# Optimization experiments

Measured on AMD Instinct MI355X. Metric: run time of the kernel, lower is better.

Reference implementation:

```python
import jax, jax.numpy as jnp
import numpy as np

EPS = 1e-5


def _bn_linear(x, g, b, W, c, relu):
    # BatchNorm1d over flattened (B*N) axis with batch statistics (training mode),
    # then Linear, then optional ReLU. x: [B, N, Din]
    mean = jnp.mean(x, axis=(0, 1))
    var = jnp.mean(jnp.square(x - mean), axis=(0, 1))  # biased variance, as torch BN uses in fwd
    xn = (x - mean) * jax.lax.rsqrt(var + EPS) * g + b
    y = jnp.einsum('bnd,od->bno', xn, W) + c
    return jax.nn.relu(y) if relu else y


def setup_inputs() -> dict:
    key = jax.random.key(0)
    ks = jax.random.split(key, 8)
    B, N = 32, 2048
    dims = [256, 512, 512, 1024]  # in_size, hidden_sizes..., out_size
    inp = {"set_feats": jax.random.normal(ks[0], (B, N, dims[0]), dtype=jnp.float32)}
    for i, (din, dout) in enumerate(zip(dims[:-1], dims[1:])):
        inp[f"g{i}"] = jnp.ones((din,), jnp.float32)
        inp[f"b{i}"] = jnp.zeros((din,), jnp.float32)
        inp[f"W{i}"] = jax.random.normal(ks[1 + i], (dout, din), dtype=jnp.float32) / np.sqrt(din)
        inp[f"c{i}"] = jax.random.normal(ks[4 + i], (dout,), dtype=jnp.float32) * 0.01
    return inp


def reference(set_feats, g0, b0, W0, c0, g1, b1, W1, c1, g2, b2, W2, c2):
    x = _bn_linear(set_feats, g0, b0, W0, c0, relu=True)
    x = _bn_linear(x, g1, b1, W1, c1, relu=True)
    x = _bn_linear(x, g2, b2, W2, c2, relu=False)
    # reduction = 'max' over the set dimension (-2)
    return jnp.max(x, axis=-2)
```

## Files before the change

### kernel.cpp

```cpp
#include <hip/hip_runtime.h>
#include <hip/hip_bf16.h>
#include <stdint.h>

typedef unsigned short u16;
typedef __attribute__((ext_vector_type(8))) __bf16 bf16x8;
typedef __attribute__((ext_vector_type(4))) float f32x4;

#define BN_EPS 1e-5f
#define MROWS 65536
#define INV_M (1.0f / 65536.0f)
#define NREP 16

__device__ __forceinline__ u16 f2bf(float f) {
  unsigned u = __builtin_bit_cast(unsigned, f);
  unsigned r = (u + 0x7FFFu + ((u >> 16) & 1u)) >> 16;
  return (u16)r;
}
__device__ __forceinline__ float bf2f(u16 h) {
  return __builtin_bit_cast(float, (unsigned)h << 16);
}

__global__ __launch_bounds__(256)
void stats_cast_k(const float* __restrict__ x, u16* __restrict__ xbf,
                  float* __restrict__ srep ) {
  const int t = threadIdx.x;
  const int tc = t & 63, tr = t >> 6;
  const int rb = blockIdx.x * 32 + tr * 8;
  float4 v[8];
#pragma unroll
  for (int i = 0; i < 8; ++i)
    v[i] = *(const float4*)(x + (size_t)(rb + i) * 256 + tc * 4);
  float s0 = 0, s1 = 0, s2 = 0, s3 = 0, q0 = 0, q1 = 0, q2 = 0, q3 = 0;
#pragma unroll
  for (int i = 0; i < 8; ++i) {
    ushort4 ov;
    ov.x = f2bf(v[i].x); ov.y = f2bf(v[i].y);
    ov.z = f2bf(v[i].z); ov.w = f2bf(v[i].w);
    *(ushort4*)(xbf + (size_t)(rb + i) * 256 + tc * 4) = ov;
    s0 += v[i].x; q0 += v[i].x * v[i].x;
    s1 += v[i].y; q1 += v[i].y * v[i].y;
    s2 += v[i].z; q2 += v[i].z * v[i].z;
    s3 += v[i].w; q3 += v[i].w * v[i].w;
  }
  __shared__ float red[4][256];
  red[tr][tc * 4 + 0] = s0; red[tr][tc * 4 + 1] = s1;
  red[tr][tc * 4 + 2] = s2; red[tr][tc * 4 + 3] = s3;
  __syncthreads();
  float* dst = srep + (blockIdx.x & (NREP - 1)) * 512;
  if (tr == 0) {
#pragma unroll
    for (int i = 0; i < 4; ++i) {
      int c = tc * 4 + i;
      atomicAdd(&dst[c], red[0][c] + red[1][c] + red[2][c] + red[3][c]);
    }
  }
  __syncthreads();
  red[tr][tc * 4 + 0] = q0; red[tr][tc * 4 + 1] = q1;
  red[tr][tc * 4 + 2] = q2; red[tr][tc * 4 + 3] = q3;
  __syncthreads();
  if (tr == 0) {
#pragma unroll
    for (int i = 0; i < 4; ++i) {
      int c = tc * 4 + i;
      atomicAdd(&dst[256 + c], red[0][c] + red[1][c] + red[2][c] + red[3][c]);
    }
  }
}

__global__ __launch_bounds__(256)
void prep_w_k(const float* __restrict__ W, const float* __restrict__ g,
              const float* __restrict__ b, const float* __restrict__ c,
              const float* __restrict__ ssum, const float* __restrict__ ssq,
              int rep_stride, int nrep,
              u16* __restrict__ Wp, float* __restrict__ cp, int din, int dout) {
  const int gw = (blockIdx.x * 256 + threadIdx.x) >> 6;
  const int l = threadIdx.x & 63;
  if (gw >= dout) return;
  const int o = gw;
  float acc = 0.f;
  for (int d0 = l * 4; d0 < din; d0 += 256) {
    float sm[4] = {}, sq[4] = {};
    for (int r = 0; r < nrep; ++r) {
      float4 a = *(const float4*)(ssum + (size_t)r * rep_stride + d0);
      float4 z = *(const float4*)(ssq + (size_t)r * rep_stride + d0);
      sm[0] += a.x; sm[1] += a.y; sm[2] += a.z; sm[3] += a.w;
      sq[0] += z.x; sq[1] += z.y; sq[2] += z.z; sq[3] += z.w;
    }
    float4 wv = *(const float4*)(W + (size_t)o * din + d0);
    float4 gv = *(const float4*)(g + d0);
    float4 bv = *(const float4*)(b + d0);
    float w4[4] = {wv.x, wv.y, wv.z, wv.w};
    float g4[4] = {gv.x, gv.y, gv.z, gv.w};
    float b4[4] = {bv.x, bv.y, bv.z, bv.w};
    ushort4 ov;
    u16 o4[4];
#pragma unroll
    for (int i = 0; i < 4; ++i) {
      float mean = sm[i] * INV_M;
      float var = sq[i] * INV_M - mean * mean;
      float alpha = g4[i] * rsqrtf(var + BN_EPS);
      float beta = b4[i] - mean * alpha;
      o4[i] = f2bf(w4[i] * alpha);
      acc += w4[i] * beta;
    }
    ov.x = o4[0]; ov.y = o4[1]; ov.z = o4[2]; ov.w = o4[3];
    *(ushort4*)(Wp + (size_t)o * din + d0) = ov;
  }
#pragma unroll
  for (int off = 32; off > 0; off >>= 1) acc += __shfl_xor(acc, off, 64);
  if (l == 0) cp[o] = c[o] + acc;
}

#define GLDS16(gp, lp) __builtin_amdgcn_global_load_lds( \
    (__attribute__((address_space(1))) void*)(void*)(gp), \
    (__attribute__((address_space(3))) void*)(lp), 16, 0, 0)

template <int KDIM, int NDIM, bool RELU, bool DOMAX>
__global__ __launch_bounds__(512, 2)
void gemm_k(const u16* __restrict__ A, const u16* __restrict__ B,
            const float* __restrict__ cp, u16* __restrict__ Y,
            float* __restrict__ osum, float* __restrict__ osq,
            unsigned* __restrict__ maxbuf) {
  constexpr int NK = KDIM >> 5;
  __shared__ __align__(16) u16 lds[8 * 8192];
  const int t = threadIdx.x;
  const int w = t >> 6, l = t & 63;
  const int lr = l & 15, lk = l >> 4;
  const int wm = w >> 2, wn = w & 3;

  const int cpx = (int)gridDim.x >> 3;
  int bid = (int)blockIdx.x;
  bid = (bid & 7) * cpx + (bid >> 3);
  constexpr int TILES_N = NDIM >> 8;
  const int tm0 = (bid / TILES_N) << 8;
  const int tn0 = (bid % TILES_N) << 8;

  const int srow = t >> 2;
  const int scol = (((t & 3) ^ ((t >> 3) & 3)) << 3);
  const u16* Ag = A + (size_t)(tm0 + srow) * KDIM + scol;
  const u16* Bg = B + (size_t)(tn0 + srow) * KDIM + scol;
  u16* const ldsA = lds;
  u16* const ldsB = lds + 4 * 8192;

#define STAGE_A(slot_, kt_) do { \
    GLDS16(Ag + (kt_) * 32, ldsA + (slot_) * 8192 + t * 8); \
    GLDS16(Ag + (size_t)128 * KDIM + (kt_) * 32, ldsA + (slot_) * 8192 + 4096 + t * 8); \
  } while (0)
#define STAGE_B(slot_, kt_) do { \
    GLDS16(Bg + (kt_) * 32, ldsB + (slot_) * 8192 + t * 8); \
    GLDS16(Bg + (size_t)128 * KDIM + (kt_) * 32, ldsB + (slot_) * 8192 + 4096 + t * 8); \
  } while (0)

  const int pc = (lk ^ ((lr >> 1) & 3)) * 8;
  const int rba = wm * 128 + lr;
  const int rbb = wn * 64 + lr;

  f32x4 acc[8][4] = {};

  STAGE_A(0, 0); STAGE_B(0, 0);
  STAGE_A(1, 1); STAGE_B(1, 1);
  STAGE_A(2, 2); STAGE_B(2, 2);
  asm volatile("s_waitcnt vmcnt(8)" ::: "memory");
  __builtin_amdgcn_s_barrier();

#pragma unroll
  for (int T = 0; T < NK; ++T) {
    const int sl = T & 3;
    const u16* la = ldsA + sl * 8192;
    const u16* lb = ldsB + sl * 8192;
    bf16x8 af[4], bf[4];
#pragma unroll
    for (int n = 0; n < 4; ++n)
      bf[n] = *(const bf16x8*)(lb + (rbb + n * 16) * 32 + pc);
#pragma unroll
    for (int j = 0; j < 4; ++j)
      af[j] = *(const bf16x8*)(la + (rba + j * 16) * 32 + pc);
    if (T + 3 < NK) STAGE_A((T + 3) & 3, T + 3);
    __builtin_amdgcn_s_barrier();
    __builtin_amdgcn_s_setprio(1);
#pragma unroll
    for (int j = 0; j < 4; ++j)
#pragma unroll
      for (int n = 0; n < 4; ++n)
        acc[j][n] = __builtin_amdgcn_mfma_f32_16x16x32_bf16(af[j], bf[n], acc[j][n], 0, 0, 0);
    __builtin_amdgcn_s_setprio(0);
#pragma unroll
    for (int j = 0; j < 4; ++j)
      af[j] = *(const bf16x8*)(la + (rba + 64 + j * 16) * 32 + pc);
    if (T + 3 < NK) STAGE_B((T + 3) & 3, T + 3);
    if (T < NK - 3)       asm volatile("s_waitcnt vmcnt(8)" ::: "memory");
    else if (T == NK - 3) asm volatile("s_waitcnt vmcnt(4)" ::: "memory");
    else if (T == NK - 2) asm volatile("s_waitcnt vmcnt(0)" ::: "memory");
    __builtin_amdgcn_s_barrier();
    __builtin_amdgcn_s_setprio(1);
#pragma unroll
    for (int j = 0; j < 4; ++j)
#pragma unroll
      for (int n = 0; n < 4; ++n)
        acc[4 + j][n] = __builtin_amdgcn_mfma_f32_16x16x32_bf16(af[j], bf[n], acc[4 + j][n], 0, 0, 0);
    __builtin_amdgcn_s_setprio(0);
  }
#undef STAGE_A
#undef STAGE_B

  if (!DOMAX) {
    float cs[4] = {}, cq[4] = {};
#pragma unroll
    for (int n = 0; n < 4; ++n) {
      const int gcol = tn0 + wn * 64 + n * 16 + lr;
      const float cb = cp[gcol];
#pragma unroll
      for (int m = 0; m < 8; ++m) {
        const int grow = tm0 + wm * 128 + m * 16 + lk * 4;
#pragma unroll
        for (int r = 0; r < 4; ++r) {
          float v = acc[m][n][r] + cb;
          if (RELU) v = fmaxf(v, 0.f);
          Y[(size_t)(grow + r) * NDIM + gcol] = f2bf(v);
          cs[n] += v;
          cq[n] += v * v;
        }
      }
    }
    if (RELU) {
#pragma unroll
      for (int n = 0; n < 4; ++n) {
        cs[n] += __shfl_xor(cs[n], 16, 64);
        cs[n] += __shfl_xor(cs[n], 32, 64);
        cq[n] += __shfl_xor(cq[n], 16, 64);
        cq[n] += __shfl_xor(cq[n], 32, 64);
      }
      float* sred = (float*)lds;
      __syncthreads();
      if (lk == 0) {
#pragma unroll
        for (int n = 0; n < 4; ++n) {
          const int c = wn * 64 + n * 16 + lr;
          sred[wm * 256 + c] = cs[n];
          sred[512 + wm * 256 + c] = cq[n];
        }
      }
      __syncthreads();
      if (t < 256) {
        atomicAdd(&osum[tn0 + t], sred[t] + sred[256 + t]);
      } else {
        const int c = t - 256;
        atomicAdd(&osq[tn0 + c], sred[512 + c] + sred[768 + c]);
      }
    }
  } else {
    const int batch = tm0 >> 11;
#pragma unroll
    for (int n = 0; n < 4; ++n) {
      const int gcol = tn0 + wn * 64 + n * 16 + lr;
      const float cb = cp[gcol];
      float mx = -3.0e38f;
#pragma unroll
      for (int m = 0; m < 8; ++m)
#pragma unroll
        for (int r = 0; r < 4; ++r)
          mx = fmaxf(mx, acc[m][n][r] + cb);
      mx = fmaxf(mx, __shfl_xor(mx, 16, 64));
      mx = fmaxf(mx, __shfl_xor(mx, 32, 64));
      if (lk == 0) {
        unsigned u = __builtin_bit_cast(unsigned, mx);
        u = (u & 0x80000000u) ? ~u : (u | 0x80000000u);
        atomicMax(&maxbuf[batch * NDIM + gcol], u);
      }
    }
  }
}

__global__ void decode_k(const unsigned* __restrict__ mb, float* __restrict__ out, int n) {
  int i = blockIdx.x * 256 + threadIdx.x;
  if (i < n) {
    unsigned u = mb[i];
    u = (u & 0x80000000u) ? (u & 0x7FFFFFFFu) : ~u;
    out[i] = __builtin_bit_cast(float, u);
  }
}

extern "C" void kernel_launch(void* const* d_in, const int* in_sizes, int n_in,
                              void* d_out, int out_size, void* d_ws, size_t ws_size,
                              hipStream_t stream) {
  const float* x0 = (const float*)d_in[0];
  const float* g0 = (const float*)d_in[1];
  const float* b0 = (const float*)d_in[2];
  const float* W0 = (const float*)d_in[3];
  const float* c0 = (const float*)d_in[4];
  const float* g1 = (const float*)d_in[5];
  const float* b1 = (const float*)d_in[6];
  const float* W1 = (const float*)d_in[7];
  const float* c1 = (const float*)d_in[8];
  const float* g2 = (const float*)d_in[9];
  const float* b2 = (const float*)d_in[10];
  const float* W2 = (const float*)d_in[11];
  const float* c2 = (const float*)d_in[12];

  char* ws = (char*)d_ws;
  size_t off = 0;
  auto alloc = [&](size_t bytes) -> char* {
    char* p = ws + off;
    off += (bytes + 255) & ~(size_t)255;
    return p;
  };
  u16* x0bf = (u16*)alloc((size_t)MROWS * 256 * 2);
  u16* y1 = (u16*)alloc((size_t)MROWS * 512 * 2);
  u16* y2 = (u16*)alloc((size_t)MROWS * 512 * 2);
  float* s0rep = (float*)alloc((NREP * 512 + 1024 + 1024 + 32768) * 4);
  float* s1sum = s0rep + NREP * 512;
  float* s1sq = s1sum + 512;
  float* s2sum = s1sum + 1024;
  float* s2sq = s2sum + 512;
  unsigned* maxbuf = (unsigned*)(s1sum + 2048);
  const size_t zbytes = (size_t)(NREP * 512 + 2048 + 32768) * 4;
  u16* W0p = (u16*)alloc(512 * 256 * 2);
  u16* W1p = (u16*)alloc(512 * 512 * 2);
  u16* W2p = (u16*)alloc(1024 * 512 * 2);
  float* c0p = (float*)alloc(512 * 4);
  float* c1p = (float*)alloc(512 * 4);
  float* c2p = (float*)alloc(1024 * 4);
  if (off > ws_size) return;

  hipMemsetAsync(s0rep, 0, zbytes, stream);

  stats_cast_k<<<2048, 256, 0, stream>>>(x0, x0bf, s0rep);
  prep_w_k<<<128, 256, 0, stream>>>(W0, g0, b0, c0, s0rep, s0rep + 256, 512, NREP,
                                    W0p, c0p, 256, 512);
  gemm_k<256, 512, true, false><<<512, 512, 0, stream>>>(x0bf, W0p, c0p, y1, s1sum, s1sq, nullptr);
  prep_w_k<<<128, 256, 0, stream>>>(W1, g1, b1, c1, s1sum, s1sq, 0, 1,
                                    W1p, c1p, 512, 512);
  gemm_k<512, 512, true, false><<<512, 512, 0, stream>>>(y1, W1p, c1p, y2, s2sum, s2sq, nullptr);
  prep_w_k<<<256, 256, 0, stream>>>(W2, g2, b2, c2, s2sum, s2sq, 0, 1,
                                    W2p, c2p, 512, 1024);
  gemm_k<512, 1024, false, true><<<1024, 512, 0, stream>>>(y2, W2p, c2p, nullptr, nullptr, nullptr, maxbuf);
  decode_k<<<128, 256, 0, stream>>>(maxbuf, (float*)d_out, 32768);
}
```

Before: 201.0 us.

## Fuse all stages into one persistent cooperative kernel with grid syncs

Replaces the memset and eight separate kernel launches with a single cooperative kernel of 256 blocks that steps through stats/cast, weight folding, three GEMMs and the max-decode, separated by grid.sync barriers. Each block now handles several GEMM tiles in sequence, and the stats pass covers more rows per block. The aim is to remove launch overhead and the idle gaps between dependent kernels. In exchange, parallelism drops to one wave of 256 blocks, the per-tile pipeline drains and refills at every tile, and the grid barriers carry their own cost.

```diff
diff --git a/kernel.cpp b/kernel.cpp
--- a/kernel.cpp
+++ b/kernel.cpp
@@ -1,6 +1,9 @@
 #include <hip/hip_runtime.h>
 #include <hip/hip_bf16.h>
+#include <hip/hip_cooperative_groups.h>
 #include <stdint.h>
+
+namespace cg = cooperative_groups;
 
 typedef unsigned short u16;
 typedef __attribute__((ext_vector_type(8))) __bf16 bf16x8;
@@ -10,71 +13,180 @@
 #define MROWS 65536
 #define INV_M (1.0f / 65536.0f)
 #define NREP 16
+#define ZWORDS (16 * 512 + 2048 + 32768)
 
 __device__ __forceinline__ u16 f2bf(float f) {
   unsigned u = __builtin_bit_cast(unsigned, f);
   unsigned r = (u + 0x7FFFu + ((u >> 16) & 1u)) >> 16;
   return (u16)r;
 }
-__device__ __forceinline__ float bf2f(u16 h) {
-  return __builtin_bit_cast(float, (unsigned)h << 16);
-}
-
-__global__ __launch_bounds__(256)
-void stats_cast_k(const float* __restrict__ x, u16* __restrict__ xbf,
-                  float* __restrict__ srep ) {
-  const int t = threadIdx.x;
-  const int tc = t & 63, tr = t >> 6;
-  const int rb = blockIdx.x * 32 + tr * 8;
-  float4 v[8];
-#pragma unroll
-  for (int i = 0; i < 8; ++i)
-    v[i] = *(const float4*)(x + (size_t)(rb + i) * 256 + tc * 4);
-  float s0 = 0, s1 = 0, s2 = 0, s3 = 0, q0 = 0, q1 = 0, q2 = 0, q3 = 0;
-#pragma unroll
-  for (int i = 0; i < 8; ++i) {
-    ushort4 ov;
-    ov.x = f2bf(v[i].x); ov.y = f2bf(v[i].y);
-    ov.z = f2bf(v[i].z); ov.w = f2bf(v[i].w);
-    *(ushort4*)(xbf + (size_t)(rb + i) * 256 + tc * 4) = ov;
-    s0 += v[i].x; q0 += v[i].x * v[i].x;
-    s1 += v[i].y; q1 += v[i].y * v[i].y;
-    s2 += v[i].z; q2 += v[i].z * v[i].z;
-    s3 += v[i].w; q3 += v[i].w * v[i].w;
+
+#define GLDS16(gp, lp) __builtin_amdgcn_global_load_lds( \
+    (__attribute__((address_space(1))) void*)(void*)(gp), \
+    (__attribute__((address_space(3))) void*)(lp), 16, 0, 0)
+
+template <int KDIM, int NDIM, bool RELU, bool DOMAX>
+__device__ __forceinline__
+void gemm_tile(const u16* __restrict__ A, const u16* __restrict__ B,
+               const float* __restrict__ cp, u16* __restrict__ Y,
+               float* __restrict__ osum, float* __restrict__ osq,
+               unsigned* __restrict__ maxbuf, int tile, u16* lds, int t) {
+  constexpr int NK = KDIM >> 5;
+  const int w = t >> 6, l = t & 63;
+  const int lr = l & 15, lk = l >> 4;
+  const int wm = w >> 2, wn = w & 3;
+  constexpr int TILES_N = NDIM >> 8;
+  const int tm0 = (tile / TILES_N) << 8;
+  const int tn0 = (tile % TILES_N) << 8;
+
+  asm volatile("s_waitcnt vmcnt(0)" ::: "memory");
+  __syncthreads();
+
+  const int srow = t >> 2;
+  const int scol = (((t & 3) ^ ((t >> 3) & 3)) << 3);
+  const u16* Ag = A + (size_t)(tm0 + srow) * KDIM + scol;
+  const u16* Bg = B + (size_t)(tn0 + srow) * KDIM + scol;
+  u16* const ldsA = lds;
+  u16* const ldsB = lds + 4 * 8192;
+
+#define STAGE_A(slot_, kt_) do { \
+    GLDS16(Ag + (kt_) * 32, ldsA + (slot_) * 8192 + t * 8); \
+    GLDS16(Ag + (size_t)128 * KDIM + (kt_) * 32, ldsA + (slot_) * 8192 + 4096 + t * 8); \
+  } while (0)
+#define STAGE_B(slot_, kt_) do { \
+    GLDS16(Bg + (kt_) * 32, ldsB + (slot_) * 8192 + t * 8); \
+    GLDS16(Bg + (size_t)128 * KDIM + (kt_) * 32, ldsB + (slot_) * 8192 + 4096 + t * 8); \
+  } while (0)
+
+  const int pc = (lk ^ ((lr >> 1) & 3)) * 8;
+  const int rba = wm * 128 + lr;
+  const int rbb = wn * 64 + lr;
+
+  f32x4 acc[8][4] = {};
+
+  STAGE_A(0, 0); STAGE_B(0, 0);
+  STAGE_A(1, 1); STAGE_B(1, 1);
+  STAGE_A(2, 2); STAGE_B(2, 2);
+  asm volatile("s_waitcnt vmcnt(8)" ::: "memory");
+  __builtin_amdgcn_s_barrier();
+
+#pragma unroll
+  for (int T = 0; T < NK; ++T) {
+    const int sl = T & 3;
+    const u16* la = ldsA + sl * 8192;
+    const u16* lb = ldsB + sl * 8192;
+    bf16x8 af[4], bf[4];
+#pragma unroll
+    for (int n = 0; n < 4; ++n)
+      bf[n] = *(const bf16x8*)(lb + (rbb + n * 16) * 32 + pc);
+#pragma unroll
+    for (int j = 0; j < 4; ++j)
+      af[j] = *(const bf16x8*)(la + (rba + j * 16) * 32 + pc);
+    if (T + 3 < NK) STAGE_A((T + 3) & 3, T + 3);
+    __builtin_amdgcn_s_barrier();
+    __builtin_amdgcn_s_setprio(1);
+#pragma unroll
+    for (int j = 0; j < 4; ++j)
+#pragma unroll
+      for (int n = 0; n < 4; ++n)
+        acc[j][n] = __builtin_amdgcn_mfma_f32_16x16x32_bf16(af[j], bf[n], acc[j][n], 0, 0, 0);
+    __builtin_amdgcn_s_setprio(0);
+#pragma unroll
+    for (int j = 0; j < 4; ++j)
+      af[j] = *(const bf16x8*)(la + (rba + 64 + j * 16) * 32 + pc);
+    if (T + 3 < NK) STAGE_B((T + 3) & 3, T + 3);
+    if (T < NK - 3)       asm volatile("s_waitcnt vmcnt(8)" ::: "memory");
+    else if (T == NK - 3) asm volatile("s_waitcnt vmcnt(4)" ::: "memory");
+    else if (T == NK - 2) asm volatile("s_waitcnt vmcnt(0)" ::: "memory");
+    __builtin_amdgcn_s_barrier();
+    __builtin_amdgcn_s_setprio(1);
+#pragma unroll
+    for (int j = 0; j < 4; ++j)
+#pragma unroll
+      for (int n = 0; n < 4; ++n)
+        acc[4 + j][n] = __builtin_amdgcn_mfma_f32_16x16x32_bf16(af[j], bf[n], acc[4 + j][n], 0, 0, 0);
+    __builtin_amdgcn_s_setprio(0);
   }
-  __shared__ float red[4][256];
-  red[tr][tc * 4 + 0] = s0; red[tr][tc * 4 + 1] = s1;
-  red[tr][tc * 4 + 2] = s2; red[tr][tc * 4 + 3] = s3;
-  __syncthreads();
-  float* dst = srep + (blockIdx.x & (NREP - 1)) * 512;
-  if (tr == 0) {
-#pragma unroll
-    for (int i = 0; i < 4; ++i) {
-      int c = tc * 4 + i;
-      atomicAdd(&dst[c], red[0][c] + red[1][c] + red[2][c] + red[3][c]);
-    }
-  }
-  __syncthreads();
-  red[tr][tc * 4 + 0] = q0; red[tr][tc * 4 + 1] = q1;
-  red[tr][tc * 4 + 2] = q2; red[tr][tc * 4 + 3] = q3;
-  __syncthreads();
-  if (tr == 0) {
-#pragma unroll
-    for (int i = 0; i < 4; ++i) {
-      int c = tc * 4 + i;
-      atomicAdd(&dst[256 + c], red[0][c] + red[1][c] + red[2][c] + red[3][c]);
+#undef STAGE_A
+#undef STAGE_B
+
+  if (!DOMAX) {
+    float cs[4] = {}, cq[4] = {};
+#pragma unroll
+    for (int n = 0; n < 4; ++n) {
+      const int gcol = tn0 + wn * 64 + n * 16 + lr;
+      const float cb = cp[gcol];
+#pragma unroll
+      for (int m = 0; m < 8; ++m) {
+        const int grow = tm0 + wm * 128 + m * 16 + lk * 4;
+#pragma unroll
+        for (int r = 0; r < 4; ++r) {
+          float v = acc[m][n][r] + cb;
+          if (RELU) v = fmaxf(v, 0.f);
+          Y[(size_t)(grow + r) * NDIM + gcol] = f2bf(v);
+          cs[n] += v;
+          cq[n] += v * v;
+        }
+      }
+    }
+    if (RELU) {
+#pragma unroll
+      for (int n = 0; n < 4; ++n) {
+        cs[n] += __shfl_xor(cs[n], 16, 64);
+        cs[n] += __shfl_xor(cs[n], 32, 64);
+        cq[n] += __shfl_xor(cq[n], 16, 64);
+        cq[n] += __shfl_xor(cq[n], 32, 64);
+      }
+      float* sred = (float*)lds;
+      __syncthreads();
+      if (lk == 0) {
+#pragma unroll
+        for (int n = 0; n < 4; ++n) {
+          const int c = wn * 64 + n * 16 + lr;
+          sred[wm * 256 + c] = cs[n];
+          sred[512 + wm * 256 + c] = cq[n];
+        }
+      }
+      __syncthreads();
+      if (t < 256) {
+        atomicAdd(&osum[tn0 + t], sred[t] + sred[256 + t]);
+      } else {
+        const int c = t - 256;
+        atomicAdd(&osq[tn0 + c], sred[512 + c] + sred[768 + c]);
+      }
+    }
+  } else {
+    const int batch = tm0 >> 11;
+#pragma unroll
+    for (int n = 0; n < 4; ++n) {
+      const int gcol = tn0 + wn * 64 + n * 16 + lr;
+      const float cb = cp[gcol];
+      float mx = -3.0e38f;
+#pragma unroll
+      for (int m = 0; m < 8; ++m)
+#pragma unroll
+        for (int r = 0; r < 4; ++r)
+          mx = fmaxf(mx, acc[m][n][r] + cb);
+      mx = fmaxf(mx, __shfl_xor(mx, 16, 64));
+      mx = fmaxf(mx, __shfl_xor(mx, 32, 64));
+      if (lk == 0) {
+        unsigned u = __builtin_bit_cast(unsigned, mx);
+        u = (u & 0x80000000u) ? ~u : (u | 0x80000000u);
+        atomicMax(&maxbuf[batch * NDIM + gcol], u);
+      }
     }
   }
 }
 
-__global__ __launch_bounds__(256)
-void prep_w_k(const float* __restrict__ W, const float* __restrict__ g,
+__device__ __forceinline__
+void prep_row(const float* __restrict__ W, const float* __restrict__ g,
               const float* __restrict__ b, const float* __restrict__ c,
               const float* __restrict__ ssum, const float* __restrict__ ssq,
               int rep_stride, int nrep,
-              u16* __restrict__ Wp, float* __restrict__ cp, int din, int dout) {
-  const int gw = (blockIdx.x * 256 + threadIdx.x) >> 6;
-  const int l = threadIdx.x & 63;
+              u16* __restrict__ Wp, float* __restrict__ cp, int din, int dout,
+              int bid, int t) {
+  const int gw = bid * 8 + (t >> 6);
+  const int l = t & 63;
   if (gw >= dout) return;
   const int o = gw;
   float acc = 0.f;
@@ -111,172 +223,123 @@
   if (l == 0) cp[o] = c[o] + acc;
 }
 
-#define GLDS16(gp, lp) __builtin_amdgcn_global_load_lds( \
-    (__attribute__((address_space(1))) void*)(void*)(gp), \
-    (__attribute__((address_space(3))) void*)(lp), 16, 0, 0)
-
-template <int KDIM, int NDIM, bool RELU, bool DOMAX>
 __global__ __launch_bounds__(512, 2)
-void gemm_k(const u16* __restrict__ A, const u16* __restrict__ B,
-            const float* __restrict__ cp, u16* __restrict__ Y,
-            float* __restrict__ osum, float* __restrict__ osq,
-            unsigned* __restrict__ maxbuf) {
-  constexpr int NK = KDIM >> 5;
+void mega_k(const float* __restrict__ x0, const float* __restrict__ g0,
+            const float* __restrict__ b0, const float* __restrict__ W0,
+            const float* __restrict__ c0, const float* __restrict__ g1,
+            const float* __restrict__ b1, const float* __restrict__ W1,
+            const float* __restrict__ c1, const float* __restrict__ g2,
+            const float* __restrict__ b2, const float* __restrict__ W2,
+            const float* __restrict__ c2,
+            u16* __restrict__ x0bf, u16* __restrict__ y1, u16* __restrict__ y2,
+            float* __restrict__ s0rep, float* __restrict__ s1sum,
+            float* __restrict__ s1sq, float* __restrict__ s2sum,
+            float* __restrict__ s2sq, unsigned* __restrict__ maxbuf,
+            u16* __restrict__ W0p, u16* __restrict__ W1p, u16* __restrict__ W2p,
+            float* __restrict__ c0p, float* __restrict__ c1p, float* __restrict__ c2p,
+            float* __restrict__ out) {
+  cg::grid_group grid = cg::this_grid();
   __shared__ __align__(16) u16 lds[8 * 8192];
-  const int t = threadIdx.x;
-  const int w = t >> 6, l = t & 63;
-  const int lr = l & 15, lk = l >> 4;
-  const int wm = w >> 2, wn = w & 3;
-
-  const int cpx = (int)gridDim.x >> 3;
-  int bid = (int)blockIdx.x;
-  bid = (bid & 7) * cpx + (bid >> 3);
-  constexpr int TILES_N = NDIM >> 8;
-  const int tm0 = (bid / TILES_N) << 8;
-  const int tn0 = (bid % TILES_N) << 8;
-
-  const int srow = t >> 2;
-  const int scol = (((t & 3) ^ ((t >> 3) & 3)) << 3);
-  const u16* Ag = A + (size_t)(tm0 + srow) * KDIM + scol;
-  const u16* Bg = B + (size_t)(tn0 + srow) * KDIM + scol;
-  u16* const ldsA = lds;
-  u16* const ldsB = lds + 4 * 8192;
-
-#define STAGE_A(slot_, kt_) do { \
-    GLDS16(Ag + (kt_) * 32, ldsA + (slot_) * 8192 + t * 8); \
-    GLDS16(Ag + (size_t)128 * KDIM + (kt_) * 32, ldsA + (slot_) * 8192 + 4096 + t * 8); \
-  } while (0)
-#define STAGE_B(slot_, kt_) do { \
-    GLDS16(Bg + (kt_) * 32, ldsB + (slot_) * 8192 + t * 8); \
-    GLDS16(Bg + (size_t)128 * KDIM + (kt_) * 32, ldsB + (slot_) * 8192 + 4096 + t * 8); \
-  } while (0)
-
-  const int pc = (lk ^ ((lr >> 1) & 3)) * 8;
-  const int rba = wm * 128 + lr;
-  const int rbb = wn * 64 + lr;
-
-  f32x4 acc[8][4] = {};
-
-  STAGE_A(0, 0); STAGE_B(0, 0);
-  STAGE_A(1, 1); STAGE_B(1, 1);
-  STAGE_A(2, 2); STAGE_B(2, 2);
-  asm volatile("s_waitcnt vmcnt(8)" ::: "memory");
-  __builtin_amdgcn_s_barrier();
-
-#pragma unroll
-  for (int T = 0; T < NK; ++T) {
-    const int sl = T & 3;
-    const u16* la = ldsA + sl * 8192;
-    const u16* lb = ldsB + sl * 8192;
-    bf16x8 af[4], bf[4];
-#pragma unroll
-    for (int n = 0; n < 4; ++n)
-      bf[n] = *(const bf16x8*)(lb + (rbb + n * 16) * 32 + pc);
-#pragma unroll
-    for (int j = 0; j < 4; ++j)
-      af[j] = *(const bf16x8*)(la + (rba + j * 16) * 32 + pc);
-    if (T + 3 < NK) STAGE_A((T + 3) & 3, T + 3);
-    __builtin_amdgcn_s_barrier();
-    __builtin_amdgcn_s_setprio(1);
-#pragma unroll
-    for (int j = 0; j < 4; ++j)
-#pragma unroll
-      for (int n = 0; n < 4; ++n)
-        acc[j][n] = __builtin_amdgcn_mfma_f32_16x16x32_bf16(af[j], bf[n], acc[j][n], 0, 0, 0);
-    __builtin_amdgcn_s_setprio(0);
-#pragma unroll
-    for (int j = 0; j < 4; ++j)
-      af[j] = *(const bf16x8*)(la + (rba + 64 + j * 16) * 32 + pc);
-    if (T + 3 < NK) STAGE_B((T + 3) & 3, T + 3);
-    if (T < NK - 3)       asm volatile("s_waitcnt vmcnt(8)" ::: "memory");
-    else if (T == NK - 3) asm volatile("s_waitcnt vmcnt(4)" ::: "memory");
-    else if (T == NK - 2) asm volatile("s_waitcnt vmcnt(0)" ::: "memory");
-    __builtin_amdgcn_s_barrier();
-    __builtin_amdgcn_s_setprio(1);
-#pragma unroll
-    for (int j = 0; j < 4; ++j)
-#pragma unroll
-      for (int n = 0; n < 4; ++n)
-        acc[4 + j][n] = __builtin_amdgcn_mfma_f32_16x16x32_bf16(af[j], bf[n], acc[4 + j][n], 0, 0, 0);
-    __builtin_amdgcn_s_setprio(0);
+  const int bid = (int)blockIdx.x;
+  const int t = (int)threadIdx.x;
+  const int swz = (bid & 7) * 32 + (bid >> 3);
+
+  for (int gid = bid * 512 + t; gid < ZWORDS; gid += 256 * 512)
+    s0rep[gid] = 0.f;
+  __threadfence();
+  grid.sync();
+
+  {
+    const int tc = t & 63, tr = t >> 6;
+    float s[4] = {}, q[4] = {};
+#pragma unroll
+    for (int pass = 0; pass < 4; ++pass) {
+      const int rb = bid * 256 + pass * 64 + tr * 8;
+      float4 v[8];
+#pragma unroll
+      for (int i = 0; i < 8; ++i)
+        v[i] = *(const float4*)(x0 + (size_t)(rb + i) * 256 + tc * 4);
+#pragma unroll
+      for (int i = 0; i < 8; ++i) {
+        ushort4 ov;
+        ov.x = f2bf(v[i].x); ov.y = f2bf(v[i].y);
+        ov.z = f2bf(v[i].z); ov.w = f2bf(v[i].w);
+        *(ushort4*)(x0bf + (size_t)(rb + i) * 256 + tc * 4) = ov;
+        s[0] += v[i].x; q[0] += v[i].x * v[i].x;
+        s[1] += v[i].y; q[1] += v[i].y * v[i].y;
+        s[2] += v[i].z; q[2] += v[i].z * v[i].z;
+        s[3] += v[i].w; q[3] += v[i].w * v[i].w;
+      }
+    }
+    float* red = (float*)lds;
+    float* dst = s0rep + (bid & (NREP - 1)) * 512;
+#pragma unroll
+    for (int i = 0; i < 4; ++i) red[tr * 256 + tc * 4 + i] = s[i];
+    __syncthreads();
+    if (tr == 0) {
+#pragma unroll
+      for (int i = 0; i < 4; ++i) {
+        const int c = tc * 4 + i;
+        float a = red[c] + red[256 + c] + red[512 + c] + red[768 + c] +
+                  red[1024 + c] + red[1280 + c] + red[1536 + c] + red[1792 + c];
+        atomicAdd(&dst[c], a);
+      }
+    }
+    __syncthreads();
+#pragma unroll
+    for (int i = 0; i < 4; ++i) red[tr * 256 + tc * 4 + i] = q[i];
+    __syncthreads();
+    if (tr == 0) {
+#pragma unroll
+      for (int i = 0; i < 4; ++i) {
+        const int c = tc * 4 + i;
+        float a = red[c] + red[256 + c] + red[512 + c] + red[768 + c] +
+                  red[1024 + c] + red[1280 + c] + red[1536 + c] + red[1792 + c];
+        atomicAdd(&dst[256 + c], a);
+      }
+    }
+    __syncthreads();
   }
-#undef STAGE_A
-#undef STAGE_B
-
-  if (!DOMAX) {
-    float cs[4] = {}, cq[4] = {};
-#pragma unroll
-    for (int n = 0; n < 4; ++n) {
-      const int gcol = tn0 + wn * 64 + n * 16 + lr;
-      const float cb = cp[gcol];
-#pragma unroll
-      for (int m = 0; m < 8; ++m) {
-        const int grow = tm0 + wm * 128 + m * 16 + lk * 4;
-#pragma unroll
-        for (int r = 0; r < 4; ++r) {
-          float v = acc[m][n][r] + cb;
-          if (RELU) v = fmaxf(v, 0.f);
-          Y[(size_t)(grow + r) * NDIM + gcol] = f2bf(v);
-          cs[n] += v;
-          cq[n] += v * v;
-        }
-      }
-    }
-    if (RELU) {
-#pragma unroll
-      for (int n = 0; n < 4; ++n) {
-        cs[n] += __shfl_xor(cs[n], 16, 64);
-        cs[n] += __shfl_xor(cs[n], 32, 64);
-        cq[n] += __shfl_xor(cq[n], 16, 64);
-        cq[n] += __shfl_xor(cq[n], 32, 64);
-      }
-      float* sred = (float*)lds;
-      __syncthreads();
-      if (lk == 0) {
-#pragma unroll
-        for (int n = 0; n < 4; ++n) {
-          const int c = wn * 64 + n * 16 + lr;
-          sred[wm * 256 + c] = cs[n];
-          sred[512 + wm * 256 + c] = cq[n];
-        }
-      }
-      __syncthreads();
-      if (t < 256) {
-        atomicAdd(&osum[tn0 + t], sred[t] + sred[256 + t]);
-      } else {
-        const int c = t - 256;
-        atomicAdd(&osq[tn0 + c], sred[512 + c] + sred[768 + c]);
-      }
-    }
-  } else {
-    const int batch = tm0 >> 11;
-#pragma unroll
-    for (int n = 0; n < 4; ++n) {
-      const int gcol = tn0 + wn * 64 + n * 16 + lr;
-      const float cb = cp[gcol];
-      float mx = -3.0e38f;
-#pragma unroll
-      for (int m = 0; m < 8; ++m)
-#pragma unroll
-        for (int r = 0; r < 4; ++r)
-          mx = fmaxf(mx, acc[m][n][r] + cb);
-      mx = fmaxf(mx, __shfl_xor(mx, 16, 64));
-      mx = fmaxf(mx, __shfl_xor(mx, 32, 64));
-      if (lk == 0) {
-        unsigned u = __builtin_bit_cast(unsigned, mx);
-        u = (u & 0x80000000u) ? ~u : (u | 0x80000000u);
-        atomicMax(&maxbuf[batch * NDIM + gcol], u);
-      }
-    }
-  }
-}
-
-__global__ void decode_k(const unsigned* __restrict__ mb, float* __restrict__ out, int n) {
-  int i = blockIdx.x * 256 + threadIdx.x;
-  if (i < n) {
-    unsigned u = mb[i];
-    u = (u & 0x80000000u) ? (u & 0x7FFFFFFFu) : ~u;
-    out[i] = __builtin_bit_cast(float, u);
+  __threadfence();
+  grid.sync();
+
+  prep_row(W0, g0, b0, c0, s0rep, s0rep + 256, 512, NREP, W0p, c0p, 256, 512, bid, t);
+  __threadfence();
+  grid.sync();
+
+  for (int r = 0; r < 2; ++r)
+    gemm_tile<256, 512, true, false>(x0bf, W0p, c0p, y1, s1sum, s1sq, nullptr,
+                                     r * 256 + swz, lds, t);
+  __threadfence();
+  grid.sync();
+
+  prep_row(W1, g1, b1, c1, s1sum, s1sq, 0, 1, W1p, c1p, 512, 512, bid, t);
+  __threadfence();
+  grid.sync();
+
+  for (int r = 0; r < 2; ++r)
+    gemm_tile<512, 512, true, false>(y1, W1p, c1p, y2, s2sum, s2sq, nullptr,
+                                     r * 256 + swz, lds, t);
+  __threadfence();
+  grid.sync();
+
+  prep_row(W2, g2, b2, c2, s2sum, s2sq, 0, 1, W2p, c2p, 512, 1024, bid, t);
+  __threadfence();
+  grid.sync();
+
+  for (int r = 0; r < 4; ++r)
+    gemm_tile<512, 1024, false, true>(y2, W2p, c2p, nullptr, nullptr, nullptr,
+                                      maxbuf, r * 256 + swz, lds, t);
+  __threadfence();
+  grid.sync();
+
+  {
+    const int gid = bid * 512 + t;
+    if (gid < 32768) {
+      unsigned u = maxbuf[gid];
+      u = (u & 0x80000000u) ? (u & 0x7FFFFFFFu) : ~u;
+      out[gid] = __builtin_bit_cast(float, u);
+    }
   }
 }
 
@@ -307,32 +370,31 @@
   u16* x0bf = (u16*)alloc((size_t)MROWS * 256 * 2);
   u16* y1 = (u16*)alloc((size_t)MROWS * 512 * 2);
   u16* y2 = (u16*)alloc((size_t)MROWS * 512 * 2);
-  float* s0rep = (float*)alloc((NREP * 512 + 1024 + 1024 + 32768) * 4);
+  float* s0rep = (float*)alloc((size_t)ZWORDS * 4);
   float* s1sum = s0rep + NREP * 512;
   float* s1sq = s1sum + 512;
   float* s2sum = s1sum + 1024;
   float* s2sq = s2sum + 512;
   unsigned* maxbuf = (unsigned*)(s1sum + 2048);
-  const size_t zbytes = (size_t)(NREP * 512 + 2048 + 32768) * 4;
   u16* W0p = (u16*)alloc(512 * 256 * 2);
   u16* W1p = (u16*)alloc(512 * 512 * 2);
   u16* W2p = (u16*)alloc(1024 * 512 * 2);
   float* c0p = (float*)alloc(512 * 4);
   float* c1p = (float*)alloc(512 * 4);
   float* c2p = (float*)alloc(1024 * 4);
+  float* outp = (float*)d_out;
   if (off > ws_size) return;
 
-  hipMemsetAsync(s0rep, 0, zbytes, stream);
-
-  stats_cast_k<<<2048, 256, 0, stream>>>(x0, x0bf, s0rep);
-  prep_w_k<<<128, 256, 0, stream>>>(W0, g0, b0, c0, s0rep, s0rep + 256, 512, NREP,
-                                    W0p, c0p, 256, 512);
-  gemm_k<256, 512, true, false><<<512, 512, 0, stream>>>(x0bf, W0p, c0p, y1, s1sum, s1sq, nullptr);
-  prep_w_k<<<128, 256, 0, stream>>>(W1, g1, b1, c1, s1sum, s1sq, 0, 1,
-                                    W1p, c1p, 512, 512);
-  gemm_k<512, 512, true, false><<<512, 512, 0, stream>>>(y1, W1p, c1p, y2, s2sum, s2sq, nullptr);
-  prep_w_k<<<256, 256, 0, stream>>>(W2, g2, b2, c2, s2sum, s2sq, 0, 1,
-                                    W2p, c2p, 512, 1024);
-  gemm_k<512, 1024, false, true><<<1024, 512, 0, stream>>>(y2, W2p, c2p, nullptr, nullptr, nullptr, maxbuf);
-  decode_k<<<128, 256, 0, stream>>>(maxbuf, (float*)d_out, 32768);
+  void* args[] = {
+    (void*)&x0, (void*)&g0, (void*)&b0, (void*)&W0, (void*)&c0,
+    (void*)&g1, (void*)&b1, (void*)&W1, (void*)&c1,
+    (void*)&g2, (void*)&b2, (void*)&W2, (void*)&c2,
+    (void*)&x0bf, (void*)&y1, (void*)&y2,
+    (void*)&s0rep, (void*)&s1sum, (void*)&s1sq, (void*)&s2sum, (void*)&s2sq,
+    (void*)&maxbuf,
+    (void*)&W0p, (void*)&W1p, (void*)&W2p,
+    (void*)&c0p, (void*)&c1p, (void*)&c2p,
+    (void*)&outp
+  };
+  hipLaunchCooperativeKernel((void*)mega_k, dim3(256), dim3(512), args, 0, stream);
 }
```

Measured after the change: 733.2 us. 3.65x slower.
